# Performance work log

Measured on AMD Instinct MI355X. Metric: run time of the kernel, lower is better.

Reference implementation:

```python
import jax, jax.numpy as jnp
import numpy as np

B, T = 64, 64
HUMAN, IN = 64, 8
HS, ES, K = 1024, 1024, 7
PSI_H, PSI_LR = 1024, 30

_PAR_SHAPES = [(HS, HS), (HS,), (IN, HS), (HS, HUMAN), (IN, HUMAN - IN)]
_PAR_SIZES = [int(np.prod(s)) for s in _PAR_SHAPES]
N_PSI = int(sum(_PAR_SIZES))
_OFFS = np.cumsum([0] + _PAR_SIZES)


def setup_inputs() -> dict:
    key = jax.random.key(0)
    ks = jax.random.split(key, 16)
    def xav(k, shape):
        lim = float(np.sqrt(6.0 / (shape[0] + shape[1])))
        return jax.random.uniform(k, shape, minval=-lim, maxval=lim, dtype=jnp.float32)
    def uni(k, shape, s):
        return jax.random.uniform(k, shape, minval=-s, maxval=s, dtype=jnp.float32)
    se = float(1.0 / np.sqrt(ES))
    return {
        "inputs": jax.random.normal(ks[0], (B, T, IN), jnp.float32),
        "outputs": jax.random.normal(ks[1], (B, T, HUMAN), jnp.float32),
        "eps": jax.random.normal(ks[2], (B, K), jnp.float32),
        "enc_Wih": uni(ks[3], (3 * ES, HUMAN), se),
        "enc_Whh": uni(ks[4], (3 * ES, ES), se),
        "enc_bih": uni(ks[5], (3 * ES,), se),
        "enc_bhh": uni(ks[6], (3 * ES,), se),
        "to_mu": xav(ks[7], (ES, K)),
        "to_lsigma": xav(ks[8], (ES, K)),
        "to_lsigma_bias": -0.5 * jnp.ones((K,), jnp.float32),
        "W1": xav(ks[9], (K, PSI_H)),
        "b1": jnp.zeros((PSI_H,), jnp.float32),
        "W2": xav(ks[10], (PSI_H, PSI_LR)),
        "b2": jnp.zeros((PSI_LR,), jnp.float32),
        "W3": xav(ks[11], (PSI_LR, N_PSI)),
        "b3": jnp.zeros((N_PSI,), jnp.float32),
        "gru_Wih": xav(ks[12], (IN, 2 * HS)),
        "gru_Whh": xav(ks[13], (HS, 2 * HS)),
        "gru_bias": jnp.concatenate([jnp.zeros((HS,)), jnp.ones((HS,))]).astype(jnp.float32),
    }


def _gru_cell(h, x, Wih, Whh, bih, bhh):
    # torch.nn.GRUCell math, gate order (r, z, n)
    gx = x @ Wih.T + bih
    gh = h @ Whh.T + bhh
    xr, xz, xn = jnp.split(gx, 3, axis=-1)
    hr, hz, hn = jnp.split(gh, 3, axis=-1)
    r = jax.nn.sigmoid(xr + hr)
    z = jax.nn.sigmoid(xz + hz)
    n = jnp.tanh(xn + r * hn)
    return (1.0 - z) * n + z * h


def _split_psi(psi):
    # psi: [B, N_PSI] -> per-sample (Whh, bh, Wih, C, D)
    return [psi[:, _OFFS[i]:_OFFS[i + 1]].reshape((-1,) + _PAR_SHAPES[i]) for i in range(5)]


def reference(inputs, outputs, eps, enc_Wih, enc_Whh, enc_bih, enc_bhh,
              to_mu, to_lsigma, to_lsigma_bias, W1, b1, W2, b2, W3, b3,
              gru_Wih, gru_Whh, gru_bias):
    bsz = inputs.shape[0]
    # ---- encoder: GRUCell over time-major outputs ----
    out_tm = jnp.swapaxes(outputs, 0, 1)  # [T, B, HUMAN]
    h0 = jnp.zeros((bsz, ES), inputs.dtype)
    h_enc = _gru_cell(h0, out_tm[0], enc_Wih, enc_Whh, enc_bih, enc_bhh)
    def enc_step(h, x):
        h = _gru_cell(h, x, enc_Wih, enc_Whh, enc_bih, enc_bhh)
        return h, None
    h_enc, _ = jax.lax.scan(enc_step, h_enc, out_tm[1:])
    mu = h_enc @ to_mu                       # [B, K]
    logstd = h_enc @ to_lsigma + to_lsigma_bias
    z = mu + eps * jnp.exp(logstd)
    # ---- hypernetwork psi decoder ----
    psi = (jnp.tanh(z @ W1 + b1) @ W2 + b2) @ W3 + b3   # [B, N_PSI]
    Whh_b, bh_b, Wih_b, C_b, D_b = _split_psi(psi)
    # ---- per-sample GRU decoder, vectorized over batch, scan over time ----
    gx_all = jnp.einsum('bti,ij->tbj', inputs, gru_Wih)  # [T, B, 2*HS]
    xW_all = jnp.einsum('bti,bih->tbh', inputs, Wih_b)   # [T, B, HS]

    def dec_step(h, xs):
        gx_t, xW_t = xs
        pre = gx_t + h @ gru_Whh + gru_bias   # [B, 2*HS]
        z_t = jax.nn.sigmoid(pre[:, :HS])
        r_t = jax.nn.sigmoid(pre[:, HS:])
        hWhh = jnp.einsum('bh,bhk->bk', h, Whh_b) + bh_b
        eta = jnp.tanh(xW_t + r_t * jnp.tanh(hWhh))
        h_new = z_t * h + (1.0 - z_t) * eta
        return h_new, h_new

    state0 = jnp.zeros((bsz, HS), inputs.dtype)
    h_last, dec_seq = jax.lax.scan(dec_step, state0, (gx_all, xW_all))
    dec_seq = jnp.swapaxes(dec_seq, 0, 1)    # [B, T, HS]
    # ---- readout ----
    yhats = jnp.einsum('bth,bhm->btm', dec_seq, C_b)
    xD = jnp.einsum('bti,bim->btm', inputs, D_b)  # [B, T, HUMAN-IN]
    yhats = yhats + jnp.concatenate([jnp.zeros_like(inputs), xD], axis=-1)
    # residual output
    yhats = yhats + jnp.concatenate(
        [inputs, jnp.zeros((bsz, inputs.shape[1], HUMAN - IN), inputs.dtype)], axis=-1)
    states = jax.lax.stop_gradient(h_last)
    return yhats, mu, logstd, states
```

## Files before the change

kernel.cpp:

```cpp
#include <hip/hip_runtime.h>

namespace {
constexpr int nT = 64;
constexpr int nK = 7;
constexpr long N_PSI = 1123776;
constexpr long SZ_WHH = 1048576;
constexpr long REST_SZ = 75200;
constexpr long R_BH = 0;
constexpr long R_WIH = 1024;
constexpr long R_C = 9216;
constexpr long R_D = 74752;
constexpr int NCH = 16;
constexpr int CHR = 64;
constexpr long PHALF = (long)NCH * 64 * 1024;
}

typedef __attribute__((ext_vector_type(4))) unsigned short us4;
typedef __attribute__((ext_vector_type(2))) unsigned short us2;

__device__ __forceinline__ float b2f(unsigned short u) {
  return __uint_as_float(((unsigned int)u) << 16);
}
__device__ __forceinline__ unsigned short f2b(float f) {
  unsigned int u = __float_as_uint(f);
  return (unsigned short)((u + 0x7fffu + ((u >> 16) & 1u)) >> 16);
}
__device__ __forceinline__ float sigm(float x) { return 1.f / (1.f + __expf(-x)); }

__global__ void transpose_bf16_k(const float* __restrict__ in, unsigned short* __restrict__ out,
                                 int rows, int cols) {
  __shared__ float tile[32][33];
  int x = blockIdx.x * 32 + threadIdx.x;
  int y = blockIdx.y * 32 + threadIdx.y;
  #pragma unroll
  for (int i = 0; i < 32; i += 8)
    if ((y + i) < rows && x < cols) tile[threadIdx.y + i][threadIdx.x] = in[(long)(y + i) * cols + x];
  __syncthreads();
  x = blockIdx.y * 32 + threadIdx.x;
  y = blockIdx.x * 32 + threadIdx.y;
  #pragma unroll
  for (int i = 0; i < 32; i += 8)
    if ((y + i) < cols && x < rows) out[(long)(y + i) * rows + x] = f2b(tile[threadIdx.x][threadIdx.y + i]);
}

__global__ void cvt_bf16_k(const float* __restrict__ in, unsigned short* __restrict__ out, long n) {
  long i = (long)blockIdx.x * 256 + threadIdx.x;
  if (i < n) out[i] = f2b(in[i]);
}

__global__ __launch_bounds__(256) void enc_gx_k(const float* __restrict__ outputs,
                                                const unsigned short* __restrict__ WtWihB,
                                                const float* __restrict__ bih,
                                                unsigned short* __restrict__ gxE) {
  int g0 = blockIdx.x * 256;
  int btg = blockIdx.y;
  __shared__ unsigned short ws[64 * 256];
  __shared__ float xs[64][64];
  for (int i = threadIdx.x; i < 64 * 256; i += 256)
    ws[i] = WtWihB[(long)(i >> 8) * 3072 + g0 + (i & 255)];
  for (int i = threadIdx.x; i < 64 * 64; i += 256) {
    int idx = btg * 64 + (i >> 6);
    int t = idx >> 6, b = idx & 63;
    xs[i >> 6][i & 63] = outputs[((long)b * nT + t) * 64 + (i & 63)];
  }
  __syncthreads();
  float bihv = bih[g0 + threadIdx.x];
  for (int j = 0; j < 64; ++j) {
    int idx = btg * 64 + j;
    float acc = bihv;
    #pragma unroll 8
    for (int i = 0; i < 64; ++i) acc += xs[j][i] * b2f(ws[i * 256 + threadIdx.x]);
    gxE[(long)idx * 3072 + g0 + threadIdx.x] = f2b(acc);
  }
}

__global__ __launch_bounds__(256) void dec_gx_k(const float* __restrict__ inputs,
                                                const float* __restrict__ gWih,
                                                const float* __restrict__ gbias,
                                                unsigned short* __restrict__ gxD) {
  int g0 = blockIdx.x * 256;
  int btg = blockIdx.y;
  __shared__ float ws[8][256];
  __shared__ float xs[64][8];
  for (int i = threadIdx.x; i < 8 * 256; i += 256)
    ws[i >> 8][i & 255] = gWih[(long)(i >> 8) * 2048 + g0 + (i & 255)];
  for (int i = threadIdx.x; i < 64 * 8; i += 256) {
    int idx = btg * 64 + (i >> 3);
    int t = idx >> 6, b = idx & 63;
    xs[i >> 3][i & 7] = inputs[((long)b * nT + t) * 8 + (i & 7)];
  }
  __syncthreads();
  float bv = gbias[g0 + threadIdx.x];
  for (int j = 0; j < 64; ++j) {
    int idx = btg * 64 + j;
    float acc = bv;
    #pragma unroll
    for (int i = 0; i < 8; ++i) acc += xs[j][i] * ws[i][threadIdx.x];
    gxD[(long)idx * 2048 + g0 + threadIdx.x] = f2b(acc);
  }
}

__global__ __launch_bounds__(256) void xW_k(const float* __restrict__ inputs,
                                            const float* __restrict__ Rest,
                                            unsigned short* __restrict__ xWb) {
  int k0 = blockIdx.x * 256;
  int b = blockIdx.y;
  __shared__ float ws[8][256];
  __shared__ float xs[64][8];
  const float* RB = Rest + (long)b * REST_SZ + R_WIH;
  for (int i = threadIdx.x; i < 8 * 256; i += 256)
    ws[i >> 8][i & 255] = RB[(long)(i >> 8) * 1024 + k0 + (i & 255)];
  for (int i = threadIdx.x; i < 64 * 8; i += 256)
    xs[i >> 3][i & 7] = inputs[((long)b * nT + (i >> 3)) * 8 + (i & 7)];
  __syncthreads();
  for (int t = 0; t < 64; ++t) {
    float acc = 0.f;
    #pragma unroll
    for (int i = 0; i < 8; ++i) acc += xs[t][i] * ws[i][threadIdx.x];
    xWb[((long)t * 64 + b) * 1024 + k0 + threadIdx.x] = f2b(acc);
  }
}

__global__ __launch_bounds__(256) void enc_step_k(
    const unsigned short* __restrict__ W,
    const unsigned short* __restrict__ gxE,
    const float* __restrict__ bhh,
    float* __restrict__ hEnc,
    const float* __restrict__ pRr, const float* __restrict__ pZr, const float* __restrict__ pNr,
    float* __restrict__ pRw, float* __restrict__ pZw, float* __restrict__ pNw,
    int t) {
  int c = blockIdx.x & (NCH - 1);
  int sp = blockIdx.x >> 4;
  int b0 = sp * 2, b1 = b0 + 1;
  __shared__ float h0s[CHR], h1s[CHR];

  int v = threadIdx.x;
  if (v < 2 * CHR) {
    int hi = v >> 6;
    int bb = hi ? b1 : b0;
    int e = c * CHR + (v & 63);
    float sr = 0.f, sz = 0.f, sn = 0.f;
    if (t > 0) {
      #pragma unroll
      for (int cc = 0; cc < NCH; ++cc) {
        long base = ((long)cc * 64 + bb) * 1024 + e;
        sr += pRr[base]; sz += pZr[base]; sn += pNr[base];
      }
    }
    long gb = ((long)t * 64 + bb) * 3072;
    float xr = b2f(gxE[gb + e]), xz = b2f(gxE[gb + 1024 + e]), xn = b2f(gxE[gb + 2048 + e]);
    float hr = sr + bhh[e], hz = sz + bhh[1024 + e], hn = sn + bhh[2048 + e];
    float r = sigm(xr + hr);
    float z = sigm(xz + hz);
    float n = tanhf(xn + r * hn);
    float hold = (t > 0) ? hEnc[(long)bb * 1024 + e] : 0.f;
    float hnew = (1.f - z) * n + z * hold;
    hEnc[(long)bb * 1024 + e] = hnew;
    if (hi) h1s[v & 63] = hnew; else h0s[v & 63] = hnew;
  }
  __syncthreads();

  if (t < nT - 1) {
    int e0 = threadIdx.x * 4;
    float ar0[4] = {}, az0[4] = {}, an0[4] = {}, ar1[4] = {}, az1[4] = {}, an1[4] = {};
    const unsigned short* Wb = W + (long)(c * CHR) * 3072 + e0;
    #pragma unroll 4
    for (int j = 0; j < CHR; ++j) {
      us4 wr = *(const us4*)(Wb + (long)j * 3072);
      us4 wz = *(const us4*)(Wb + (long)j * 3072 + 1024);
      us4 wn = *(const us4*)(Wb + (long)j * 3072 + 2048);
      float hv0 = h0s[j], hv1 = h1s[j];
      #pragma unroll
      for (int q = 0; q < 4; ++q) {
        float fr = b2f(wr[q]), fz = b2f(wz[q]), fn = b2f(wn[q]);
        ar0[q] += hv0 * fr; az0[q] += hv0 * fz; an0[q] += hv0 * fn;
        ar1[q] += hv1 * fr; az1[q] += hv1 * fz; an1[q] += hv1 * fn;
      }
    }
    long i0 = ((long)c * 64 + b0) * 1024 + e0;
    long i1 = i0 + 1024;
    *(float4*)(pRw + i0) = make_float4(ar0[0], ar0[1], ar0[2], ar0[3]);
    *(float4*)(pZw + i0) = make_float4(az0[0], az0[1], az0[2], az0[3]);
    *(float4*)(pNw + i0) = make_float4(an0[0], an0[1], an0[2], an0[3]);
    *(float4*)(pRw + i1) = make_float4(ar1[0], ar1[1], ar1[2], ar1[3]);
    *(float4*)(pZw + i1) = make_float4(az1[0], az1[1], az1[2], az1[3]);
    *(float4*)(pNw + i1) = make_float4(an1[0], an1[1], an1[2], an1[3]);
  }
}

__global__ __launch_bounds__(256) void latent_hyper_k(
    const float* __restrict__ h_enc,
    const float* __restrict__ to_mu, const float* __restrict__ to_lsig,
    const float* __restrict__ lsig_bias, const float* __restrict__ eps,
    const float* __restrict__ W1, const float* __restrict__ b1,
    const float* __restrict__ W2, const float* __restrict__ b2,
    float* __restrict__ out_mu, float* __restrict__ out_lsig,
    float* __restrict__ a2out) {
  int b = blockIdx.x;
  __shared__ float hs[1024];
  __shared__ float zv[8];
  __shared__ float a1[1024];
  for (int i = threadIdx.x; i < 1024; i += 256) hs[i] = h_enc[b * 1024 + i];
  __syncthreads();
  int g = threadIdx.x >> 5, s = threadIdx.x & 31;
  if (g < nK) {
    float am = 0.f, as_ = 0.f;
    for (int h = s; h < 1024; h += 32) {
      float hv = hs[h];
      am += hv * to_mu[h * nK + g];
      as_ += hv * to_lsig[h * nK + g];
    }
    #pragma unroll
    for (int m = 16; m >= 1; m >>= 1) { am += __shfl_xor(am, m); as_ += __shfl_xor(as_, m); }
    if (s == 0) {
      float ls = as_ + lsig_bias[g];
      out_mu[b * nK + g] = am;
      out_lsig[b * nK + g] = ls;
      zv[g] = am + eps[b * nK + g] * __expf(ls);
    }
  }
  __syncthreads();
  for (int j = threadIdx.x; j < 1024; j += 256) {
    float acc = b1[j];
    #pragma unroll
    for (int i = 0; i < nK; ++i) acc += zv[i] * W1[i * 1024 + j];
    a1[j] = tanhf(acc);
  }
  __syncthreads();
  int l = threadIdx.x >> 3, s8 = threadIdx.x & 7;
  if (l < 30) {
    float acc = 0.f;
    for (int j = s8; j < 1024; j += 8) acc += a1[j] * W2[j * 30 + l];
    acc += __shfl_xor(acc, 4);
    acc += __shfl_xor(acc, 2);
    acc += __shfl_xor(acc, 1);
    if (s8 == 0) a2out[b * 30 + l] = acc + b2[l];
  }
}

__global__ __launch_bounds__(256) void psi_k(const float* __restrict__ a2,
                                             const float* __restrict__ W3, const float* __restrict__ b3,
                                             unsigned short* __restrict__ WhhB, float* __restrict__ Rest) {
  __shared__ float sa[64 * 30];
  for (int i = threadIdx.x; i < 64 * 30; i += 256) sa[i] = a2[i];
  long n0 = ((long)blockIdx.x * 256 + threadIdx.x) * 2;
  __syncthreads();
  if (n0 >= N_PSI) return;
  float2 w[30];
  #pragma unroll
  for (int l = 0; l < 30; ++l) w[l] = *(const float2*)(W3 + (long)l * N_PSI + n0);
  float2 bb = *(const float2*)(b3 + n0);
  bool isWhh = (n0 < SZ_WHH);
  for (int b = 0; b < 64; ++b) {
    float a0 = bb.x, a1v = bb.y;
    const float* ab = &sa[b * 30];
    #pragma unroll
    for (int l = 0; l < 30; ++l) { float av = ab[l]; a0 += av * w[l].x; a1v += av * w[l].y; }
    if (isWhh) {
      us2 o; o[0] = f2b(a0); o[1] = f2b(a1v);
      *(us2*)(WhhB + (long)b * SZ_WHH + n0) = o;
    } else {
      *(float2*)(Rest + (long)b * REST_SZ + (n0 - SZ_WHH)) = make_float2(a0, a1v);
    }
  }
}

__global__ __launch_bounds__(256) void wmax_k(const unsigned short* __restrict__ WhhB,
                                              float* __restrict__ pmax) {
  int b = blockIdx.x >> 2, rq = blockIdx.x & 3;
  int k0 = threadIdx.x * 4;
  float m0 = 0.f, m1 = 0.f, m2 = 0.f, m3 = 0.f;
  const unsigned short* W = WhhB + (long)b * SZ_WHH + (long)rq * 256 * 1024 + k0;
  #pragma unroll 4
  for (int j = 0; j < 256; ++j) {
    us4 w = *(const us4*)(W + (long)j * 1024);
    m0 = fmaxf(m0, fabsf(b2f(w[0])));
    m1 = fmaxf(m1, fabsf(b2f(w[1])));
    m2 = fmaxf(m2, fabsf(b2f(w[2])));
    m3 = fmaxf(m3, fabsf(b2f(w[3])));
  }
  *(float4*)(pmax + ((long)b * 4 + rq) * 1024 + k0) = make_float4(m0, m1, m2, m3);
}

__global__ __launch_bounds__(256) void wscale_k(const float* __restrict__ pmax,
                                                float* __restrict__ wsc) {
  int b = blockIdx.x;
  int k0 = threadIdx.x * 4;
  float4 a = *(const float4*)(pmax + ((long)b * 4 + 0) * 1024 + k0);
  float4 c = *(const float4*)(pmax + ((long)b * 4 + 1) * 1024 + k0);
  float4 d = *(const float4*)(pmax + ((long)b * 4 + 2) * 1024 + k0);
  float4 e = *(const float4*)(pmax + ((long)b * 4 + 3) * 1024 + k0);
  float m0 = fmaxf(fmaxf(a.x, c.x), fmaxf(d.x, e.x));
  float m1 = fmaxf(fmaxf(a.y, c.y), fmaxf(d.y, e.y));
  float m2 = fmaxf(fmaxf(a.z, c.z), fmaxf(d.z, e.z));
  float m3 = fmaxf(fmaxf(a.w, c.w), fmaxf(d.w, e.w));
  float s0 = (m0 > 0.f) ? m0 / 127.f : 1.f;
  float s1 = (m1 > 0.f) ? m1 / 127.f : 1.f;
  float s2 = (m2 > 0.f) ? m2 / 127.f : 1.f;
  float s3 = (m3 > 0.f) ? m3 / 127.f : 1.f;
  *(float4*)(wsc + (long)b * 1024 + k0) = make_float4(s0, s1, s2, s3);
}

__global__ __launch_bounds__(256) void wquant_k(const unsigned short* __restrict__ WhhB,
                                                const float* __restrict__ wsc,
                                                char* __restrict__ Q8) {
  int b = blockIdx.x >> 2, rq = blockIdx.x & 3;
  int k0 = threadIdx.x * 4;
  float4 s = *(const float4*)(wsc + (long)b * 1024 + k0);
  float i0 = 1.f / s.x, i1 = 1.f / s.y, i2 = 1.f / s.z, i3 = 1.f / s.w;
  const unsigned short* W = WhhB + (long)b * SZ_WHH + (long)rq * 256 * 1024 + k0;
  char* Q = Q8 + (long)b * SZ_WHH + (long)rq * 256 * 1024 + k0;
  #pragma unroll 4
  for (int j = 0; j < 256; ++j) {
    us4 w = *(const us4*)(W + (long)j * 1024);
    int q0 = __float2int_rn(b2f(w[0]) * i0);
    int q1 = __float2int_rn(b2f(w[1]) * i1);
    int q2 = __float2int_rn(b2f(w[2]) * i2);
    int q3 = __float2int_rn(b2f(w[3]) * i3);
    q0 = min(127, max(-127, q0)); q1 = min(127, max(-127, q1));
    q2 = min(127, max(-127, q2)); q3 = min(127, max(-127, q3));
    *(char4*)(Q + (long)j * 1024) = make_char4((char)q0, (char)q1, (char)q2, (char)q3);
  }
}

__global__ __launch_bounds__(256) void dec_step_q8_k(
    const char* __restrict__ Q8,
    const float* __restrict__ Wsc,
    const unsigned short* __restrict__ gWhhB,
    const unsigned short* __restrict__ gxD,
    const unsigned short* __restrict__ xWb,
    const float* __restrict__ Rest,
    float* __restrict__ decS,
    const float* __restrict__ pZr, const float* __restrict__ pRr, const float* __restrict__ pWr,
    float* __restrict__ pZw, float* __restrict__ pRw, float* __restrict__ pWw,
    int t) {
  int c = blockIdx.x & (NCH - 1);
  int sp = blockIdx.x >> 4;
  int b0 = sp * 2, b1 = b0 + 1;
  __shared__ float h0s[CHR], h1s[CHR];

  int v = threadIdx.x;
  if (v < 2 * CHR) {
    int hi = v >> 6;
    int bb = hi ? b1 : b0;
    int k = c * CHR + (v & 63);
    float sz = 0.f, sr = 0.f, sw = 0.f;
    float hold = 0.f;
    if (t > 0) {
      #pragma unroll
      for (int cc = 0; cc < NCH; ++cc) {
        long base = ((long)cc * 64 + bb) * 1024 + k;
        sz += pZr[base]; sr += pRr[base]; sw += pWr[base];
      }
      hold = decS[((long)bb * nT + (t - 1)) * 1024 + k];
    }
    long gb = ((long)t * 64 + bb) * 2048;
    float gz = b2f(gxD[gb + k]), gr = b2f(gxD[gb + 1024 + k]);
    float z = sigm(gz + sz);
    float r = sigm(gr + sr);
    float hW = sw + Rest[(long)bb * REST_SZ + R_BH + k];
    float xw = b2f(xWb[((long)t * 64 + bb) * 1024 + k]);
    float eta = tanhf(xw + r * tanhf(hW));
    float hnew = z * hold + (1.f - z) * eta;
    decS[((long)bb * nT + t) * 1024 + k] = hnew;
    if (hi) h1s[v & 63] = hnew; else h0s[v & 63] = hnew;
  }
  __syncthreads();

  if (t < nT - 1) {
    int k0 = threadIdx.x * 4;
    float az0[4] = {}, ar0[4] = {}, aw0[4] = {}, az1[4] = {}, ar1[4] = {}, aw1[4] = {};
    const unsigned short* G = gWhhB + (long)(c * CHR) * 2048 + k0;
    const char* Q0 = Q8 + (long)b0 * SZ_WHH + (long)(c * CHR) * 1024 + k0;
    const char* Q1 = Q8 + (long)b1 * SZ_WHH + (long)(c * CHR) * 1024 + k0;
    #pragma unroll 4
    for (int j = 0; j < CHR; ++j) {
      us4 wz = *(const us4*)(G + (long)j * 2048);
      us4 wr = *(const us4*)(G + (long)j * 2048 + 1024);
      char4 q0 = *(const char4*)(Q0 + (long)j * 1024);
      char4 q1 = *(const char4*)(Q1 + (long)j * 1024);
      float hv0 = h0s[j], hv1 = h1s[j];
      float f00 = (float)q0.x, f01 = (float)q0.y, f02 = (float)q0.z, f03 = (float)q0.w;
      float f10 = (float)q1.x, f11 = (float)q1.y, f12 = (float)q1.z, f13 = (float)q1.w;
      #pragma unroll
      for (int q = 0; q < 4; ++q) {
        float fz = b2f(wz[q]), fr = b2f(wr[q]);
        az0[q] += hv0 * fz; ar0[q] += hv0 * fr;
        az1[q] += hv1 * fz; ar1[q] += hv1 * fr;
      }
      aw0[0] += hv0 * f00; aw0[1] += hv0 * f01; aw0[2] += hv0 * f02; aw0[3] += hv0 * f03;
      aw1[0] += hv1 * f10; aw1[1] += hv1 * f11; aw1[2] += hv1 * f12; aw1[3] += hv1 * f13;
    }
    float4 s0v = *(const float4*)(Wsc + (long)b0 * 1024 + k0);
    float4 s1v = *(const float4*)(Wsc + (long)b1 * 1024 + k0);
    aw0[0] *= s0v.x; aw0[1] *= s0v.y; aw0[2] *= s0v.z; aw0[3] *= s0v.w;
    aw1[0] *= s1v.x; aw1[1] *= s1v.y; aw1[2] *= s1v.z; aw1[3] *= s1v.w;
    long i0 = ((long)c * 64 + b0) * 1024 + k0;
    long i1 = i0 + 1024;
    *(float4*)(pZw + i0) = make_float4(az0[0], az0[1], az0[2], az0[3]);
    *(float4*)(pRw + i0) = make_float4(ar0[0], ar0[1], ar0[2], ar0[3]);
    *(float4*)(pWw + i0) = make_float4(aw0[0], aw0[1], aw0[2], aw0[3]);
    *(float4*)(pZw + i1) = make_float4(az1[0], az1[1], az1[2], az1[3]);
    *(float4*)(pRw + i1) = make_float4(ar1[0], ar1[1], ar1[2], ar1[3]);
    *(float4*)(pWw + i1) = make_float4(aw1[0], aw1[1], aw1[2], aw1[3]);
  }
}

__global__ __launch_bounds__(256) void dec_step_bf_k(
    const unsigned short* __restrict__ WhhB,
    const unsigned short* __restrict__ gWhhB,
    const unsigned short* __restrict__ gxD,
    const unsigned short* __restrict__ xWb,
    const float* __restrict__ Rest,
    float* __restrict__ decS,
    const float* __restrict__ pZr, const float* __restrict__ pRr, const float* __restrict__ pWr,
    float* __restrict__ pZw, float* __restrict__ pRw, float* __restrict__ pWw,
    int t) {
  int c = blockIdx.x & (NCH - 1);
  int sp = blockIdx.x >> 4;
  int b0 = sp * 2, b1 = b0 + 1;
  __shared__ float h0s[CHR], h1s[CHR];

  int v = threadIdx.x;
  if (v < 2 * CHR) {
    int hi = v >> 6;
    int bb = hi ? b1 : b0;
    int k = c * CHR + (v & 63);
    float sz = 0.f, sr = 0.f, sw = 0.f;
    float hold = 0.f;
    if (t > 0) {
      #pragma unroll
      for (int cc = 0; cc < NCH; ++cc) {
        long base = ((long)cc * 64 + bb) * 1024 + k;
        sz += pZr[base]; sr += pRr[base]; sw += pWr[base];
      }
      hold = decS[((long)bb * nT + (t - 1)) * 1024 + k];
    }
    long gb = ((long)t * 64 + bb) * 2048;
    float gz = b2f(gxD[gb + k]), gr = b2f(gxD[gb + 1024 + k]);
    float z = sigm(gz + sz);
    float r = sigm(gr + sr);
    float hW = sw + Rest[(long)bb * REST_SZ + R_BH + k];
    float xw = b2f(xWb[((long)t * 64 + bb) * 1024 + k]);
    float eta = tanhf(xw + r * tanhf(hW));
    float hnew = z * hold + (1.f - z) * eta;
    decS[((long)bb * nT + t) * 1024 + k] = hnew;
    if (hi) h1s[v & 63] = hnew; else h0s[v & 63] = hnew;
  }
  __syncthreads();

  if (t < nT - 1) {
    int k0 = threadIdx.x * 4;
    float az0[4] = {}, ar0[4] = {}, aw0[4] = {}, az1[4] = {}, ar1[4] = {}, aw1[4] = {};
    const unsigned short* G = gWhhB + (long)(c * CHR) * 2048 + k0;
    const unsigned short* W0 = WhhB + (long)b0 * SZ_WHH + (long)(c * CHR) * 1024 + k0;
    const unsigned short* W1p = WhhB + (long)b1 * SZ_WHH + (long)(c * CHR) * 1024 + k0;
    #pragma unroll 4
    for (int j = 0; j < CHR; ++j) {
      us4 wz = *(const us4*)(G + (long)j * 2048);
      us4 wr = *(const us4*)(G + (long)j * 2048 + 1024);
      us4 w0 = *(const us4*)(W0 + (long)j * 1024);
      us4 w1 = *(const us4*)(W1p + (long)j * 1024);
      float hv0 = h0s[j], hv1 = h1s[j];
      #pragma unroll
      for (int q = 0; q < 4; ++q) {
        float fz = b2f(wz[q]), fr = b2f(wr[q]), f0 = b2f(w0[q]), f1 = b2f(w1[q]);
        az0[q] += hv0 * fz; ar0[q] += hv0 * fr; aw0[q] += hv0 * f0;
        az1[q] += hv1 * fz; ar1[q] += hv1 * fr; aw1[q] += hv1 * f1;
      }
    }
    long i0 = ((long)c * 64 + b0) * 1024 + k0;
    long i1 = i0 + 1024;
    *(float4*)(pZw + i0) = make_float4(az0[0], az0[1], az0[2], az0[3]);
    *(float4*)(pRw + i0) = make_float4(ar0[0], ar0[1], ar0[2], ar0[3]);
    *(float4*)(pWw + i0) = make_float4(aw0[0], aw0[1], aw0[2], aw0[3]);
    *(float4*)(pZw + i1) = make_float4(az1[0], az1[1], az1[2], az1[3]);
    *(float4*)(pRw + i1) = make_float4(ar1[0], ar1[1], ar1[2], ar1[3]);
    *(float4*)(pWw + i1) = make_float4(aw1[0], aw1[1], aw1[2], aw1[3]);
  }
}

__global__ __launch_bounds__(256) void readout_k(
    const float* __restrict__ dec_seq, const float* __restrict__ inputs,
    const float* __restrict__ Rest, float* __restrict__ yhats) {
  int b = blockIdx.x >> 3;
  int tg = blockIdx.x & 7;
  __shared__ float ss[8][1024];
  __shared__ float part[4][8][64];
  for (int i = threadIdx.x; i < 8 * 1024; i += 256)
    ss[i >> 10][i & 1023] = dec_seq[((long)b * nT + tg * 8 + (i >> 10)) * 1024 + (i & 1023)];
  __syncthreads();
  int m = threadIdx.x & 63, hq = threadIdx.x >> 6;
  const float* C = Rest + (long)b * REST_SZ + R_C;
  float acc[8] = {};
  for (int h = hq * 256; h < hq * 256 + 256; ++h) {
    float cv = C[(long)h * 64 + m];
    #pragma unroll
    for (int tt = 0; tt < 8; ++tt) acc[tt] += ss[tt][h] * cv;
  }
  #pragma unroll
  for (int tt = 0; tt < 8; ++tt) part[hq][tt][m] = acc[tt];
  __syncthreads();
  const float* D = Rest + (long)b * REST_SZ + R_D;
  for (int o = threadIdx.x; o < 512; o += 256) {
    int tt = o >> 6, mm = o & 63;
    float a = part[0][tt][mm] + part[1][tt][mm] + part[2][tt][mm] + part[3][tt][mm];
    long bt = (long)b * nT + tg * 8 + tt;
    if (mm < 8) {
      a += inputs[bt * 8 + mm];
    } else {
      #pragma unroll
      for (int i = 0; i < 8; ++i) a += inputs[bt * 8 + i] * D[i * 56 + (mm - 8)];
    }
    yhats[bt * 64 + mm] = a;
  }
}

__global__ void copy_states_k(const float* __restrict__ dec_seq, float* __restrict__ states) {
  int i = blockIdx.x * 256 + threadIdx.x;
  int b = i >> 10, h = i & 1023;
  states[i] = dec_seq[((long)b * nT + (nT - 1)) * 1024 + h];
}

extern "C" void kernel_launch(void* const* d_in, const int* in_sizes, int n_in,
                              void* d_out, int out_size, void* d_ws, size_t ws_size,
                              hipStream_t stream) {
  const float* inputs  = (const float*)d_in[0];
  const float* outputs = (const float*)d_in[1];
  const float* eps     = (const float*)d_in[2];
  const float* enc_Wih = (const float*)d_in[3];
  const float* enc_Whh = (const float*)d_in[4];
  const float* enc_bih = (const float*)d_in[5];
  const float* enc_bhh = (const float*)d_in[6];
  const float* to_mu   = (const float*)d_in[7];
  const float* to_lsig = (const float*)d_in[8];
  const float* lsig_b  = (const float*)d_in[9];
  const float* W1 = (const float*)d_in[10];
  const float* b1 = (const float*)d_in[11];
  const float* W2 = (const float*)d_in[12];
  const float* b2 = (const float*)d_in[13];
  const float* W3 = (const float*)d_in[14];
  const float* b3 = (const float*)d_in[15];
  const float* gWih  = (const float*)d_in[16];
  const float* gWhh  = (const float*)d_in[17];
  const float* gbias = (const float*)d_in[18];

  char* ws = (char*)d_ws;
  size_t off = 0;
  auto alloc = [&](size_t bytes) { size_t o = off; off = (off + bytes + 255) & ~(size_t)255; return o; };
  size_t oWhhB   = alloc(64ull * SZ_WHH * 2);
  size_t oRest   = alloc(64ull * REST_SZ * 4);
  size_t ogWhhB  = alloc(1024ull * 2048 * 2);
  size_t oWtWhhB = alloc(1024ull * 3072 * 2);
  size_t oWtWihB = alloc(64ull * 3072 * 2);
  size_t ogxE    = alloc(64ull * 64 * 3072 * 2);
  size_t ogxD    = alloc(64ull * 64 * 2048 * 2);
  size_t oxWb    = alloc(64ull * 64 * 1024 * 2);
  size_t opA     = alloc((size_t)2 * PHALF * 4);
  size_t opB     = alloc((size_t)2 * PHALF * 4);
  size_t opC     = alloc((size_t)2 * PHALF * 4);
  size_t ohA     = alloc(64ull * 1024 * 4);
  size_t oDec    = alloc(64ull * 64 * 1024 * 4);
  size_t oA2     = alloc(64 * 30 * 4);
  size_t oQ8     = alloc(64ull * SZ_WHH);
  size_t oPmax   = alloc(64ull * 4 * 1024 * 4);
  size_t oWsc    = alloc(64ull * 1024 * 4);
  bool useQ8 = (off <= ws_size);
  (void)in_sizes; (void)n_in; (void)out_size;

  unsigned short* WhhB   = (unsigned short*)(ws + oWhhB);
  float*          Rest   = (float*)(ws + oRest);
  unsigned short* gWhhB  = (unsigned short*)(ws + ogWhhB);
  unsigned short* WtWhhB = (unsigned short*)(ws + oWtWhhB);
  unsigned short* WtWihB = (unsigned short*)(ws + oWtWihB);
  unsigned short* gxE    = (unsigned short*)(ws + ogxE);
  unsigned short* gxD    = (unsigned short*)(ws + ogxD);
  unsigned short* xWb    = (unsigned short*)(ws + oxWb);
  float* pA   = (float*)(ws + opA);
  float* pB   = (float*)(ws + opB);
  float* pC   = (float*)(ws + opC);
  float* hA   = (float*)(ws + ohA);
  float* decS = (float*)(ws + oDec);
  float* a2   = (float*)(ws + oA2);
  char*  Q8   = (char*)(ws + oQ8);
  float* pmax = (float*)(ws + oPmax);
  float* wsc  = (float*)(ws + oWsc);

  float* out    = (float*)d_out;
  float* out_yh = out;
  float* out_mu = out + 262144;
  float* out_ls = out + 262144 + 448;
  float* out_st = out + 262144 + 896;

  transpose_bf16_k<<<dim3(32, 96), dim3(32, 8), 0, stream>>>(enc_Whh, WtWhhB, 3072, 1024);
  transpose_bf16_k<<<dim3(2, 96),  dim3(32, 8), 0, stream>>>(enc_Wih, WtWihB, 3072, 64);
  cvt_bf16_k<<<(int)((1024ull * 2048 + 255) / 256), 256, 0, stream>>>(gWhh, gWhhB, 1024 * 2048);

  enc_gx_k<<<dim3(12, 64), 256, 0, stream>>>(outputs, WtWihB, enc_bih, gxE);

  for (int t = 0; t < nT; ++t) {
    int rp = t & 1, wp = (t + 1) & 1;
    enc_step_k<<<512, 256, 0, stream>>>(WtWhhB, gxE, enc_bhh, hA,
        pA + (size_t)rp * PHALF, pB + (size_t)rp * PHALF, pC + (size_t)rp * PHALF,
        pA + (size_t)wp * PHALF, pB + (size_t)wp * PHALF, pC + (size_t)wp * PHALF, t);
  }

  latent_hyper_k<<<64, 256, 0, stream>>>(hA, to_mu, to_lsig, lsig_b, eps,
                                         W1, b1, W2, b2, out_mu, out_ls, a2);
  psi_k<<<(int)((N_PSI / 2 + 255) / 256), 256, 0, stream>>>(a2, W3, b3, WhhB, Rest);

  if (useQ8) {
    wmax_k<<<256, 256, 0, stream>>>(WhhB, pmax);
    wscale_k<<<64, 256, 0, stream>>>(pmax, wsc);
    wquant_k<<<256, 256, 0, stream>>>(WhhB, wsc, Q8);
  }

  dec_gx_k<<<dim3(8, 64), 256, 0, stream>>>(inputs, gWih, gbias, gxD);
  xW_k<<<dim3(4, 64), 256, 0, stream>>>(inputs, Rest, xWb);

  for (int t = 0; t < nT; ++t) {
    int rp = t & 1, wp = (t + 1) & 1;
    if (useQ8) {
      dec_step_q8_k<<<512, 256, 0, stream>>>(Q8, wsc, gWhhB, gxD, xWb, Rest, decS,
          pA + (size_t)rp * PHALF, pB + (size_t)rp * PHALF, pC + (size_t)rp * PHALF,
          pA + (size_t)wp * PHALF, pB + (size_t)wp * PHALF, pC + (size_t)wp * PHALF, t);
    } else {
      dec_step_bf_k<<<512, 256, 0, stream>>>(WhhB, gWhhB, gxD, xWb, Rest, decS,
          pA + (size_t)rp * PHALF, pB + (size_t)rp * PHALF, pC + (size_t)rp * PHALF,
          pA + (size_t)wp * PHALF, pB + (size_t)wp * PHALF, pC + (size_t)wp * PHALF, t);
    }
  }

  readout_k<<<512, 256, 0, stream>>>(decS, inputs, Rest, out_yh);
  copy_states_k<<<256, 256, 0, stream>>>(decS, out_st);
}
```

Baseline: 2.989 ms.

## Split recurrent step blocks into gate roles and double the grid

Each encoder and decoder step kernel now launches twice as many blocks. One role computes the r/z gate partial matvecs and the other computes the n (or per-sample Whh) partial, and both redundantly recompute the elementwise state update. The encoder hidden state is ping-ponged between two buffers so duplicate blocks never race on read-after-write. The goal is more parallelism and memory-level concurrency per latency-bound step, at the cost of duplicated gate math and partial-sum reads. The bf16 fallback decoder path is removed, so the int8 path is assumed to always fit in the workspace.

```diff
diff --git a/kernel.cpp b/kernel.cpp
--- a/kernel.cpp
+++ b/kernel.cpp
@@ -121,16 +121,17 @@
   }
 }
 
-__global__ __launch_bounds__(256) void enc_step_k(
+__global__ __launch_bounds__(256) void enc_step2_k(
     const unsigned short* __restrict__ W,
     const unsigned short* __restrict__ gxE,
     const float* __restrict__ bhh,
-    float* __restrict__ hEnc,
+    const float* __restrict__ hIn, float* __restrict__ hOut,
     const float* __restrict__ pRr, const float* __restrict__ pZr, const float* __restrict__ pNr,
     float* __restrict__ pRw, float* __restrict__ pZw, float* __restrict__ pNw,
     int t) {
-  int c = blockIdx.x & (NCH - 1);
-  int sp = blockIdx.x >> 4;
+  int role = blockIdx.x & 1;
+  int c = (blockIdx.x >> 1) & (NCH - 1);
+  int sp = blockIdx.x >> 5;
   int b0 = sp * 2, b1 = b0 + 1;
   __shared__ float h0s[CHR], h1s[CHR];
 
@@ -153,38 +154,54 @@
     float r = sigm(xr + hr);
     float z = sigm(xz + hz);
     float n = tanhf(xn + r * hn);
-    float hold = (t > 0) ? hEnc[(long)bb * 1024 + e] : 0.f;
+    float hold = (t > 0) ? hIn[(long)bb * 1024 + e] : 0.f;
     float hnew = (1.f - z) * n + z * hold;
-    hEnc[(long)bb * 1024 + e] = hnew;
+    if (role == 0) hOut[(long)bb * 1024 + e] = hnew;
     if (hi) h1s[v & 63] = hnew; else h0s[v & 63] = hnew;
   }
   __syncthreads();
 
   if (t < nT - 1) {
     int e0 = threadIdx.x * 4;
-    float ar0[4] = {}, az0[4] = {}, an0[4] = {}, ar1[4] = {}, az1[4] = {}, an1[4] = {};
-    const unsigned short* Wb = W + (long)(c * CHR) * 3072 + e0;
-    #pragma unroll 4
-    for (int j = 0; j < CHR; ++j) {
-      us4 wr = *(const us4*)(Wb + (long)j * 3072);
-      us4 wz = *(const us4*)(Wb + (long)j * 3072 + 1024);
-      us4 wn = *(const us4*)(Wb + (long)j * 3072 + 2048);
-      float hv0 = h0s[j], hv1 = h1s[j];
-      #pragma unroll
-      for (int q = 0; q < 4; ++q) {
-        float fr = b2f(wr[q]), fz = b2f(wz[q]), fn = b2f(wn[q]);
-        ar0[q] += hv0 * fr; az0[q] += hv0 * fz; an0[q] += hv0 * fn;
-        ar1[q] += hv1 * fr; az1[q] += hv1 * fz; an1[q] += hv1 * fn;
+    if (role == 0) {
+      float ar0[4] = {}, az0[4] = {}, ar1[4] = {}, az1[4] = {};
+      const unsigned short* Wb = W + (long)(c * CHR) * 3072 + e0;
+      #pragma unroll 4
+      for (int j = 0; j < CHR; ++j) {
+        us4 wr = *(const us4*)(Wb + (long)j * 3072);
+        us4 wz = *(const us4*)(Wb + (long)j * 3072 + 1024);
+        float hv0 = h0s[j], hv1 = h1s[j];
+        #pragma unroll
+        for (int q = 0; q < 4; ++q) {
+          float fr = b2f(wr[q]), fz = b2f(wz[q]);
+          ar0[q] += hv0 * fr; az0[q] += hv0 * fz;
+          ar1[q] += hv1 * fr; az1[q] += hv1 * fz;
+        }
       }
-    }
-    long i0 = ((long)c * 64 + b0) * 1024 + e0;
-    long i1 = i0 + 1024;
-    *(float4*)(pRw + i0) = make_float4(ar0[0], ar0[1], ar0[2], ar0[3]);
-    *(float4*)(pZw + i0) = make_float4(az0[0], az0[1], az0[2], az0[3]);
-    *(float4*)(pNw + i0) = make_float4(an0[0], an0[1], an0[2], an0[3]);
-    *(float4*)(pRw + i1) = make_float4(ar1[0], ar1[1], ar1[2], ar1[3]);
-    *(float4*)(pZw + i1) = make_float4(az1[0], az1[1], az1[2], az1[3]);
-    *(float4*)(pNw + i1) = make_float4(an1[0], an1[1], an1[2], an1[3]);
+      long i0 = ((long)c * 64 + b0) * 1024 + e0;
+      long i1 = i0 + 1024;
+      *(float4*)(pRw + i0) = make_float4(ar0[0], ar0[1], ar0[2], ar0[3]);
+      *(float4*)(pZw + i0) = make_float4(az0[0], az0[1], az0[2], az0[3]);
+      *(float4*)(pRw + i1) = make_float4(ar1[0], ar1[1], ar1[2], ar1[3]);
+      *(float4*)(pZw + i1) = make_float4(az1[0], az1[1], az1[2], az1[3]);
+    } else {
+      float an0[4] = {}, an1[4] = {};
+      const unsigned short* Wb = W + (long)(c * CHR) * 3072 + 2048 + e0;
+      #pragma unroll 8
+      for (int j = 0; j < CHR; ++j) {
+        us4 wn = *(const us4*)(Wb + (long)j * 3072);
+        float hv0 = h0s[j], hv1 = h1s[j];
+        #pragma unroll
+        for (int q = 0; q < 4; ++q) {
+          float fn = b2f(wn[q]);
+          an0[q] += hv0 * fn; an1[q] += hv1 * fn;
+        }
+      }
+      long i0 = ((long)c * 64 + b0) * 1024 + e0;
+      long i1 = i0 + 1024;
+      *(float4*)(pNw + i0) = make_float4(an0[0], an0[1], an0[2], an0[3]);
+      *(float4*)(pNw + i1) = make_float4(an1[0], an1[1], an1[2], an1[3]);
+    }
   }
 }
 
@@ -323,7 +340,7 @@
   }
 }
 
-__global__ __launch_bounds__(256) void dec_step_q8_k(
+__global__ __launch_bounds__(256) void dec_step_q8b_k(
     const char* __restrict__ Q8,
     const float* __restrict__ Wsc,
     const unsigned short* __restrict__ gWhhB,
@@ -334,8 +351,9 @@
     const float* __restrict__ pZr, const float* __restrict__ pRr, const float* __restrict__ pWr,
     float* __restrict__ pZw, float* __restrict__ pRw, float* __restrict__ pWw,
     int t) {
-  int c = blockIdx.x & (NCH - 1);
-  int sp = blockIdx.x >> 4;
+  int role = blockIdx.x & 1;
+  int c = (blockIdx.x >> 1) & (NCH - 1);
+  int sp = blockIdx.x >> 5;
   int b0 = sp * 2, b1 = b0 + 1;
   __shared__ float h0s[CHR], h1s[CHR];
 
@@ -362,121 +380,57 @@
     float xw = b2f(xWb[((long)t * 64 + bb) * 1024 + k]);
     float eta = tanhf(xw + r * tanhf(hW));
     float hnew = z * hold + (1.f - z) * eta;
-    decS[((long)bb * nT + t) * 1024 + k] = hnew;
+    if (role == 0) decS[((long)bb * nT + t) * 1024 + k] = hnew;
     if (hi) h1s[v & 63] = hnew; else h0s[v & 63] = hnew;
   }
   __syncthreads();
 
   if (t < nT - 1) {
     int k0 = threadIdx.x * 4;
-    float az0[4] = {}, ar0[4] = {}, aw0[4] = {}, az1[4] = {}, ar1[4] = {}, aw1[4] = {};
-    const unsigned short* G = gWhhB + (long)(c * CHR) * 2048 + k0;
-    const char* Q0 = Q8 + (long)b0 * SZ_WHH + (long)(c * CHR) * 1024 + k0;
-    const char* Q1 = Q8 + (long)b1 * SZ_WHH + (long)(c * CHR) * 1024 + k0;
-    #pragma unroll 4
-    for (int j = 0; j < CHR; ++j) {
-      us4 wz = *(const us4*)(G + (long)j * 2048);
-      us4 wr = *(const us4*)(G + (long)j * 2048 + 1024);
-      char4 q0 = *(const char4*)(Q0 + (long)j * 1024);
-      char4 q1 = *(const char4*)(Q1 + (long)j * 1024);
-      float hv0 = h0s[j], hv1 = h1s[j];
-      float f00 = (float)q0.x, f01 = (float)q0.y, f02 = (float)q0.z, f03 = (float)q0.w;
-      float f10 = (float)q1.x, f11 = (float)q1.y, f12 = (float)q1.z, f13 = (float)q1.w;
-      #pragma unroll
-      for (int q = 0; q < 4; ++q) {
-        float fz = b2f(wz[q]), fr = b2f(wr[q]);
-        az0[q] += hv0 * fz; ar0[q] += hv0 * fr;
-        az1[q] += hv1 * fz; ar1[q] += hv1 * fr;
+    if (role == 0) {
+      float az0[4] = {}, ar0[4] = {}, az1[4] = {}, ar1[4] = {};
+      const unsigned short* G = gWhhB + (long)(c * CHR) * 2048 + k0;
+      #pragma unroll 4
+      for (int j = 0; j < CHR; ++j) {
+        us4 wz = *(const us4*)(G + (long)j * 2048);
+        us4 wr = *(const us4*)(G + (long)j * 2048 + 1024);
+        float hv0 = h0s[j], hv1 = h1s[j];
+        #pragma unroll
+        for (int q = 0; q < 4; ++q) {
+          float fz = b2f(wz[q]), fr = b2f(wr[q]);
+          az0[q] += hv0 * fz; ar0[q] += hv0 * fr;
+          az1[q] += hv1 * fz; ar1[q] += hv1 * fr;
+        }
       }
-      aw0[0] += hv0 * f00; aw0[1] += hv0 * f01; aw0[2] += hv0 * f02; aw0[3] += hv0 * f03;
-      aw1[0] += hv1 * f10; aw1[1] += hv1 * f11; aw1[2] += hv1 * f12; aw1[3] += hv1 * f13;
-    }
-    float4 s0v = *(const float4*)(Wsc + (long)b0 * 1024 + k0);
-    float4 s1v = *(const float4*)(Wsc + (long)b1 * 1024 + k0);
-    aw0[0] *= s0v.x; aw0[1] *= s0v.y; aw0[2] *= s0v.z; aw0[3] *= s0v.w;
-    aw1[0] *= s1v.x; aw1[1] *= s1v.y; aw1[2] *= s1v.z; aw1[3] *= s1v.w;
-    long i0 = ((long)c * 64 + b0) * 1024 + k0;
-    long i1 = i0 + 1024;
-    *(float4*)(pZw + i0) = make_float4(az0[0], az0[1], az0[2], az0[3]);
-    *(float4*)(pRw + i0) = make_float4(ar0[0], ar0[1], ar0[2], ar0[3]);
-    *(float4*)(pWw + i0) = make_float4(aw0[0], aw0[1], aw0[2], aw0[3]);
-    *(float4*)(pZw + i1) = make_float4(az1[0], az1[1], az1[2], az1[3]);
-    *(float4*)(pRw + i1) = make_float4(ar1[0], ar1[1], ar1[2], ar1[3]);
-    *(float4*)(pWw + i1) = make_float4(aw1[0], aw1[1], aw1[2], aw1[3]);
-  }
-}
-
-__global__ __launch_bounds__(256) void dec_step_bf_k(
-    const unsigned short* __restrict__ WhhB,
-    const unsigned short* __restrict__ gWhhB,
-    const unsigned short* __restrict__ gxD,
-    const unsigned short* __restrict__ xWb,
-    const float* __restrict__ Rest,
-    float* __restrict__ decS,
-    const float* __restrict__ pZr, const float* __restrict__ pRr, const float* __restrict__ pWr,
-    float* __restrict__ pZw, float* __restrict__ pRw, float* __restrict__ pWw,
-    int t) {
-  int c = blockIdx.x & (NCH - 1);
-  int sp = blockIdx.x >> 4;
-  int b0 = sp * 2, b1 = b0 + 1;
-  __shared__ float h0s[CHR], h1s[CHR];
-
-  int v = threadIdx.x;
-  if (v < 2 * CHR) {
-    int hi = v >> 6;
-    int bb = hi ? b1 : b0;
-    int k = c * CHR + (v & 63);
-    float sz = 0.f, sr = 0.f, sw = 0.f;
-    float hold = 0.f;
-    if (t > 0) {
-      #pragma unroll
-      for (int cc = 0; cc < NCH; ++cc) {
-        long base = ((long)cc * 64 + bb) * 1024 + k;
-        sz += pZr[base]; sr += pRr[base]; sw += pWr[base];
+      long i0 = ((long)c * 64 + b0) * 1024 + k0;
+      long i1 = i0 + 1024;
+      *(float4*)(pZw + i0) = make_float4(az0[0], az0[1], az0[2], az0[3]);
+      *(float4*)(pRw + i0) = make_float4(ar0[0], ar0[1], ar0[2], ar0[3]);
+      *(float4*)(pZw + i1) = make_float4(az1[0], az1[1], az1[2], az1[3]);
+      *(float4*)(pRw + i1) = make_float4(ar1[0], ar1[1], ar1[2], ar1[3]);
+    } else {
+      float aw0[4] = {}, aw1[4] = {};
+      const char* Q0 = Q8 + (long)b0 * SZ_WHH + (long)(c * CHR) * 1024 + k0;
+      const char* Q1 = Q8 + (long)b1 * SZ_WHH + (long)(c * CHR) * 1024 + k0;
+      #pragma unroll 8
+      for (int j = 0; j < CHR; ++j) {
+        char4 q0 = *(const char4*)(Q0 + (long)j * 1024);
+        char4 q1 = *(const char4*)(Q1 + (long)j * 1024);
+        float hv0 = h0s[j], hv1 = h1s[j];
+        aw0[0] += hv0 * (float)q0.x; aw0[1] += hv0 * (float)q0.y;
+        aw0[2] += hv0 * (float)q0.z; aw0[3] += hv0 * (float)q0.w;
+        aw1[0] += hv1 * (float)q1.x; aw1[1] += hv1 * (float)q1.y;
+        aw1[2] += hv1 * (float)q1.z; aw1[3] += hv1 * (float)q1.w;
       }
-      hold = decS[((long)bb * nT + (t - 1)) * 1024 + k];
-    }
-    long gb = ((long)t * 64 + bb) * 2048;
-    float gz = b2f(gxD[gb + k]), gr = b2f(gxD[gb + 1024 + k]);
-    float z = sigm(gz + sz);
-    float r = sigm(gr + sr);
-    float hW = sw + Rest[(long)bb * REST_SZ + R_BH + k];
-    float xw = b2f(xWb[((long)t * 64 + bb) * 1024 + k]);
-    float eta = tanhf(xw + r * tanhf(hW));
-    float hnew = z * hold + (1.f - z) * eta;
-    decS[((long)bb * nT + t) * 1024 + k] = hnew;
-    if (hi) h1s[v & 63] = hnew; else h0s[v & 63] = hnew;
-  }
-  __syncthreads();
-
-  if (t < nT - 1) {
-    int k0 = threadIdx.x * 4;
-    float az0[4] = {}, ar0[4] = {}, aw0[4] = {}, az1[4] = {}, ar1[4] = {}, aw1[4] = {};
-    const unsigned short* G = gWhhB + (long)(c * CHR) * 2048 + k0;
-    const unsigned short* W0 = WhhB + (long)b0 * SZ_WHH + (long)(c * CHR) * 1024 + k0;
-    const unsigned short* W1p = WhhB + (long)b1 * SZ_WHH + (long)(c * CHR) * 1024 + k0;
-    #pragma unroll 4
-    for (int j = 0; j < CHR; ++j) {
-      us4 wz = *(const us4*)(G + (long)j * 2048);
-      us4 wr = *(const us4*)(G + (long)j * 2048 + 1024);
-      us4 w0 = *(const us4*)(W0 + (long)j * 1024);
-      us4 w1 = *(const us4*)(W1p + (long)j * 1024);
-      float hv0 = h0s[j], hv1 = h1s[j];
-      #pragma unroll
-      for (int q = 0; q < 4; ++q) {
-        float fz = b2f(wz[q]), fr = b2f(wr[q]), f0 = b2f(w0[q]), f1 = b2f(w1[q]);
-        az0[q] += hv0 * fz; ar0[q] += hv0 * fr; aw0[q] += hv0 * f0;
-        az1[q] += hv1 * fz; ar1[q] += hv1 * fr; aw1[q] += hv1 * f1;
-      }
-    }
-    long i0 = ((long)c * 64 + b0) * 1024 + k0;
-    long i1 = i0 + 1024;
-    *(float4*)(pZw + i0) = make_float4(az0[0], az0[1], az0[2], az0[3]);
-    *(float4*)(pRw + i0) = make_float4(ar0[0], ar0[1], ar0[2], ar0[3]);
-    *(float4*)(pWw + i0) = make_float4(aw0[0], aw0[1], aw0[2], aw0[3]);
-    *(float4*)(pZw + i1) = make_float4(az1[0], az1[1], az1[2], az1[3]);
-    *(float4*)(pRw + i1) = make_float4(ar1[0], ar1[1], ar1[2], ar1[3]);
-    *(float4*)(pWw + i1) = make_float4(aw1[0], aw1[1], aw1[2], aw1[3]);
+      float4 s0v = *(const float4*)(Wsc + (long)b0 * 1024 + k0);
+      float4 s1v = *(const float4*)(Wsc + (long)b1 * 1024 + k0);
+      aw0[0] *= s0v.x; aw0[1] *= s0v.y; aw0[2] *= s0v.z; aw0[3] *= s0v.w;
+      aw1[0] *= s1v.x; aw1[1] *= s1v.y; aw1[2] *= s1v.z; aw1[3] *= s1v.w;
+      long i0 = ((long)c * 64 + b0) * 1024 + k0;
+      long i1 = i0 + 1024;
+      *(float4*)(pWw + i0) = make_float4(aw0[0], aw0[1], aw0[2], aw0[3]);
+      *(float4*)(pWw + i1) = make_float4(aw1[0], aw1[1], aw1[2], aw1[3]);
+    }
   }
 }
 
@@ -560,6 +514,7 @@
   size_t opB     = alloc((size_t)2 * PHALF * 4);
   size_t opC     = alloc((size_t)2 * PHALF * 4);
   size_t ohA     = alloc(64ull * 1024 * 4);
+  size_t ohB     = alloc(64ull * 1024 * 4);
   size_t oDec    = alloc(64ull * 64 * 1024 * 4);
   size_t oA2     = alloc(64 * 30 * 4);
   size_t oQ8     = alloc(64ull * SZ_WHH);
@@ -580,6 +535,7 @@
   float* pB   = (float*)(ws + opB);
   float* pC   = (float*)(ws + opC);
   float* hA   = (float*)(ws + ohA);
+  float* hB   = (float*)(ws + ohB);
   float* decS = (float*)(ws + oDec);
   float* a2   = (float*)(ws + oA2);
   char*  Q8   = (char*)(ws + oQ8);
@@ -600,7 +556,9 @@
 
   for (int t = 0; t < nT; ++t) {
     int rp = t & 1, wp = (t + 1) & 1;
-    enc_step_k<<<512, 256, 0, stream>>>(WtWhhB, gxE, enc_bhh, hA,
+    const float* hIn = (t & 1) ? hB : hA;
+    float* hOut      = ((t + 1) & 1) ? hB : hA;
+    enc_step2_k<<<1024, 256, 0, stream>>>(WtWhhB, gxE, enc_bhh, hIn, hOut,
         pA + (size_t)rp * PHALF, pB + (size_t)rp * PHALF, pC + (size_t)rp * PHALF,
         pA + (size_t)wp * PHALF, pB + (size_t)wp * PHALF, pC + (size_t)wp * PHALF, t);
   }
@@ -620,15 +578,9 @@
 
   for (int t = 0; t < nT; ++t) {
     int rp = t & 1, wp = (t + 1) & 1;
-    if (useQ8) {
-      dec_step_q8_k<<<512, 256, 0, stream>>>(Q8, wsc, gWhhB, gxD, xWb, Rest, decS,
-          pA + (size_t)rp * PHALF, pB + (size_t)rp * PHALF, pC + (size_t)rp * PHALF,
-          pA + (size_t)wp * PHALF, pB + (size_t)wp * PHALF, pC + (size_t)wp * PHALF, t);
-    } else {
-      dec_step_bf_k<<<512, 256, 0, stream>>>(WhhB, gWhhB, gxD, xWb, Rest, decS,
-          pA + (size_t)rp * PHALF, pB + (size_t)rp * PHALF, pC + (size_t)rp * PHALF,
-          pA + (size_t)wp * PHALF, pB + (size_t)wp * PHALF, pC + (size_t)wp * PHALF, t);
-    }
+    dec_step_q8b_k<<<1024, 256, 0, stream>>>(Q8, wsc, gWhhB, gxD, xWb, Rest, decS,
+        pA + (size_t)rp * PHALF, pB + (size_t)rp * PHALF, pC + (size_t)rp * PHALF,
+        pA + (size_t)wp * PHALF, pB + (size_t)wp * PHALF, pC + (size_t)wp * PHALF, t);
   }
 
   readout_k<<<512, 256, 0, stream>>>(decS, inputs, Rest, out_yh);
```

Measured after the change: 3.185 ms. 1.07x slower.
